# Optimization experiments

Hardware: AMD Instinct MI355X
Metric: run time of the kernel (lower is better)

The kernel has to match this reference:

```python
import jax, jax.numpy as jnp
import numpy as np

VECT = 300   # word-vector dim
H = 128      # GRU hidden size
NSTACK = 3   # MultiHead stacks (shared SelfAttention weights)
SEQ = 4096


def _ln(x, g, b, eps=1e-5):
    m = jnp.mean(x, axis=-1, keepdims=True)
    v = jnp.mean((x - m) ** 2, axis=-1, keepdims=True)
    return g * (x - m) / jnp.sqrt(v + eps) + b


def _multihead(x, q_w, q_b, k_w, k_b, v_w, v_b, aln_g, aln_b, w_w, w_b, mln_g, mln_b):
    # x: [S, 300]. Same attention weights reused for all 3 stacks (as in source).
    scale = jnp.sqrt(jnp.asarray(float(VECT), x.dtype))
    out = x
    for _ in range(NSTACK):
        q = out @ q_w.T + q_b
        k = out @ k_w.T + k_b
        v = out @ v_w.T + v_b
        a = jax.nn.softmax((q @ k.T) / scale, axis=1)      # [S, S]
        h = _ln(a @ v + out, aln_g, aln_b)                  # SelfAttention out
        out = _ln(h @ w_w.T + w_b + x, mln_g, mln_b)        # residual to original x
    return out


def _gru(xs, w_ih, w_hh, b_ih, b_hh):
    # xs: [S, VECT]; PyTorch GRUCell math, h0 = zeros. Input projections batched.
    gx = xs @ w_ih.T + b_ih  # [S, 3H]
    def step(h, g):
        gh = h @ w_hh.T + b_hh
        r = jax.nn.sigmoid(g[:H] + gh[:H])
        z = jax.nn.sigmoid(g[H:2 * H] + gh[H:2 * H])
        n = jnp.tanh(g[2 * H:] + r * gh[2 * H:])
        return (1.0 - z) * n + z * h, None
    h, _ = jax.lax.scan(step, jnp.zeros((H,), xs.dtype), gx)
    return h


def setup_inputs() -> dict:
    key = jax.random.key(0)
    ks = jax.random.split(key, 16)

    def lin(k, o, i, s=0.05):
        k1, k2 = jax.random.split(k)
        return (jax.random.normal(k1, (o, i), jnp.float32) * s,
                jax.random.normal(k2, (o,), jnp.float32) * s)

    q_w, q_b = lin(ks[0], VECT, VECT)
    k_w, k_b = lin(ks[1], VECT, VECT)
    v_w, v_b = lin(ks[2], VECT, VECT)
    w_w, w_b = lin(ks[3], VECT, VECT)
    g1_wih, g1_bih = lin(ks[4], 3 * H, VECT)
    g1_whh, g1_bhh = lin(ks[5], 3 * H, H)
    g2_wih, g2_bih = lin(ks[6], 3 * H, VECT)
    g2_whh, g2_bhh = lin(ks[7], 3 * H, H)
    fc1_w, fc1_b = lin(ks[8], 256, 2 * H)
    fc2_w, fc2_b = lin(ks[9], 3, 256)

    return {
        'x1': jax.random.normal(ks[10], (SEQ, VECT), jnp.float32),
        'x2': jax.random.normal(ks[11], (SEQ, VECT), jnp.float32),
        'q_w': q_w, 'q_b': q_b, 'k_w': k_w, 'k_b': k_b, 'v_w': v_w, 'v_b': v_b,
        'aln_g': jnp.ones((VECT,), jnp.float32), 'aln_b': jnp.zeros((VECT,), jnp.float32),
        'w_w': w_w, 'w_b': w_b,
        'mln_g': jnp.ones((VECT,), jnp.float32), 'mln_b': jnp.zeros((VECT,), jnp.float32),
        'g1_wih': g1_wih, 'g1_whh': g1_whh, 'g1_bih': g1_bih, 'g1_bhh': g1_bhh,
        'g2_wih': g2_wih, 'g2_whh': g2_whh, 'g2_bih': g2_bih, 'g2_bhh': g2_bhh,
        'fc1_w': fc1_w, 'fc1_b': fc1_b, 'fc2_w': fc2_w, 'fc2_b': fc2_b,
    }


def reference(x1, x2, q_w, q_b, k_w, k_b, v_w, v_b, aln_g, aln_b, w_w, w_b,
              mln_g, mln_b, g1_wih, g1_whh, g1_bih, g1_bhh,
              g2_wih, g2_whh, g2_bih, g2_bhh, fc1_w, fc1_b, fc2_w, fc2_b):
    a1 = _multihead(x1, q_w, q_b, k_w, k_b, v_w, v_b, aln_g, aln_b, w_w, w_b, mln_g, mln_b)
    a2 = _multihead(x2, q_w, q_b, k_w, k_b, v_w, v_b, aln_g, aln_b, w_w, w_b, mln_g, mln_b)
    h1 = _gru(a1, g1_wih, g1_whh, g1_bih, g1_bhh)  # [H]
    h2 = _gru(a2, g2_wih, g2_whh, g2_bih, g2_bhh)  # [H]
    h = jnp.concatenate([h1, h2])[None, :]          # [1, 2H]
    h = jax.nn.relu(h @ fc1_w.T + fc1_b)
    return jax.nn.log_softmax(h @ fc2_w.T + fc2_b, axis=1)  # [1, 3]
```

## Files before the change

kernel.cpp:

```cpp
#include <hip/hip_runtime.h>
#include <hip/hip_bf16.h>

#define SEQL 4096
#define VECT 300
#define DP   320
#define NQT  20
#define HN   128
#define G3   384
#define JC   4
#define KROW 328
#define VROW 40
#define PROW 40

typedef unsigned short u16;
typedef unsigned char  u8;
typedef __attribute__((ext_vector_type(8))) short bf16x8;
typedef __attribute__((ext_vector_type(4))) float f32x4;
typedef __attribute__((ext_vector_type(4))) unsigned int u32x4;
typedef __attribute__((ext_vector_type(8))) int   v8i;

#define MFMA(a,b,c) __builtin_amdgcn_mfma_f32_16x16x32_bf16(a,b,c,0,0,0)

#define L2E 1.44269504088896f

__device__ __forceinline__ float bf2f(u16 v){
    union { unsigned u; float f; } t; t.u = ((unsigned)v) << 16; return t.f;
}
__device__ __forceinline__ u16 f2bf(float f){
    union { float f; unsigned u; } t; t.f = f;
    return (u16)((t.u + 0x7FFFu + ((t.u >> 16) & 1u)) >> 16);
}
__device__ __forceinline__ float sigm_f(float x){
    return __builtin_amdgcn_rcpf(1.f + __builtin_amdgcn_exp2f(-L2E * x));
}
__device__ __forceinline__ float tanh_f(float x){
    return fmaf(2.f, __builtin_amdgcn_rcpf(1.f + __builtin_amdgcn_exp2f(-2.f * L2E * x)), -1.f);
}
__device__ __forceinline__ float sel4(f32x4 v, int r){
    float a = (r & 1) ? v.y : v.x;
    float b = (r & 1) ? v.w : v.z;
    return (r & 2) ? b : a;
}

__global__ __launch_bounds__(256) void cvt_pad(const float* __restrict__ src,
                                               u16* __restrict__ dst,
                                               int R, int C, int Rp, int Cp, float scale)
{
    int n = Rp * Cp;
    for (int i = blockIdx.x * blockDim.x + threadIdx.x; i < n; i += gridDim.x * blockDim.x){
        int r = i / Cp, c = i - r * Cp;
        float v = (r < R && c < C) ? src[r * C + c] * scale : 0.f;
        dst[i] = f2bf(v);
    }
}

__global__ __launch_bounds__(256) void cvt_whh(const float* __restrict__ src,
                                               u8* __restrict__ dst)
{
    int idx = blockIdx.x * 256 + threadIdx.x;
    if (idx >= G3 * HN) return;
    int prow = idx >> 7, col = idx & 127;
    int w  = prow / 96, rem = prow - w * 96;
    int tg = rem / 48;  rem -= tg * 48;
    int g  = rem >> 4;  int rr = rem & 15;
    int orow = g * 128 + w * 32 + tg * 16 + rr;
    int pk = __builtin_amdgcn_cvt_pk_fp8_f32(src[orow * HN + col], 0.f, 0, false);
    dst[idx] = (u8)(pk & 0xFF);
}

__global__ __launch_bounds__(256) void scale_copy(const float* __restrict__ src,
                                                  float* __restrict__ dst, int n, float scale)
{
    int i = blockIdx.x * blockDim.x + threadIdx.x;
    if (i < n) dst[i] = src[i] * scale;
}

__global__ __launch_bounds__(256) void pad_x(const float* __restrict__ src,
                                             float* __restrict__ xf, u16* __restrict__ cur)
{
    int n = SEQL * DP;
    for (int i = blockIdx.x * blockDim.x + threadIdx.x; i < n; i += gridDim.x * blockDim.x){
        int r = i / DP, c = i - r * DP;
        float v = (c < VECT) ? src[r * VECT + c] : 0.f;
        xf[i]  = v;
        cur[i] = f2bf(v);
    }
}

template<int NT, int OM, bool WPERSEQ>
__global__ __launch_bounds__(256) void gemm_k(
    const u16* __restrict__ A, const u16* __restrict__ Wp,
    const float* __restrict__ b0, const float* __restrict__ b1, const float* __restrict__ b2,
    int nb, void* __restrict__ Out)
{
    const int lane = threadIdx.x & 63;
    const int wid  = threadIdx.x >> 6;
    const int s    = blockIdx.z;
    const int sl   = blockIdx.y;
    const int wsel = WPERSEQ ? s : sl;
    const int row0 = blockIdx.x * 64 + wid * 16;
    const int m    = lane & 15;
    const int q    = lane >> 4;

    const u16* Arow = A + ((long)s * SEQL + row0) * DP;
    const u16* W    = Wp + (long)wsel * (NT * 16) * DP;

    f32x4 zf = {0.f, 0.f, 0.f, 0.f};
    f32x4 acc[NT];
    #pragma unroll
    for (int n = 0; n < NT; n++) acc[n] = zf;

    for (int c = 0; c < DP / 32; ++c){
        const int koff = c * 32 + q * 8;
        bf16x8 a0 = *(const bf16x8*)(Arow + m * DP + koff);
        #pragma unroll
        for (int n = 0; n < NT; n++){
            bf16x8 b = *(const bf16x8*)(W + (n * 16 + m) * DP + koff);
            acc[n] = MFMA(a0, b, acc[n]);
        }
    }

    const int bsel = WPERSEQ ? s : sl;
    const float* bp = (bsel == 0) ? b0 : ((bsel == 1) ? b1 : b2);
    const long SLC = 2L * SEQL * DP;

    #pragma unroll
    for (int n = 0; n < NT; n++){
        int col = n * 16 + m;
        float bv = (col < nb) ? bp[col] : 0.f;
        #pragma unroll
        for (int r = 0; r < 4; r++){
            long row = row0 + q * 4 + r;
            float v = acc[n][r] + bv;
            if (OM == 1){
                long off = ((long)s * SEQL + row) * (long)(NT * 16) + col;
                ((float*)Out)[off] = v;
            } else if (OM == 4){
                int g = col >> 7, i2 = col & 127;
                long off = ((long)s * SEQL + row) * (long)(NT * 16) + (i2 * 3 + g);
                ((float*)Out)[off] = v;
            } else {
                long off;
                if (sl < 2) off = ((long)(sl * 2 + s) * SEQL + row) * DP + col;
                else        off = 2 * SLC + ((long)s * DP + col) * SEQL + row;
                ((u16*)Out)[off] = f2bf(v);
            }
        }
    }
}

__global__ __launch_bounds__(256, 1) void flash_k(
    const u16* __restrict__ Q, const u16* __restrict__ K, const u16* __restrict__ VT,
    u16* __restrict__ Onum, float* __restrict__ Lp)
{
    const int tid  = threadIdx.x;
    const int lane = tid & 63;
    const int wid  = tid >> 6;
    const int bid  = blockIdx.x;
    const int s    = bid & 1;
    const int jc   = (bid >> 1) & 3;
    const int xi   = bid >> 3;
    const int row0 = xi * 128 + wid * 32;
    const int m = lane & 15, q = lane >> 4;

    __shared__ __align__(16) u16 Kt[32 * KROW];
    __shared__ __align__(16) u16 Vt[DP * VROW];
    __shared__ __align__(16) u16 pb[4][2][16 * PROW];

    const u16* Qb = Q  + ((long)s * SEQL + row0) * DP;
    const u16* Kc = K  + (long)s * SEQL * DP + (long)jc * 1024 * DP;
    const u16* Vc = VT + (long)s * DP * SEQL + jc * 1024;

    bf16x8 qf0[10], qf1[10];
    #pragma unroll
    for (int c = 0; c < 10; c++){
        qf0[c] = *(const bf16x8*)(Qb + (m     ) * DP + c * 32 + q * 8);
        qf1[c] = *(const bf16x8*)(Qb + (m + 16) * DP + c * 32 + q * 8);
    }

    int skoff[5], wkoff[5], svoff[5], wvoff[5];
    #pragma unroll
    for (int it = 0; it < 5; it++){
        int f  = (it * 256 + tid) * 8;
        int rk = f / 320, ck = f - rk * 320;
        skoff[it] = f;
        wkoff[it] = rk * KROW + ck;
        int rv = f >> 5, cv = f & 31;
        svoff[it] = rv * SEQL + cv;
        wvoff[it] = rv * VROW + cv;
    }

    f32x4 zf = {0.f, 0.f, 0.f, 0.f};
    f32x4 oacc0[NQT], oacc1[NQT];
    #pragma unroll
    for (int n = 0; n < NQT; n++){ oacc0[n] = zf; oacc1[n] = zf; }
    float lacc0[4] = {0,0,0,0}, lacc1[4] = {0,0,0,0};

    const float K2 = 0.057735026918962576f * L2E;
    const float MB = -16.f * L2E;

    u32x4 kreg[5], vreg[5];
    #pragma unroll
    for (int it = 0; it < 5; it++){
        kreg[it] = *(const u32x4*)(Kc + skoff[it]);
        vreg[it] = *(const u32x4*)(Vc + svoff[it]);
    }
    #pragma unroll
    for (int it = 0; it < 5; it++){
        *(u32x4*)(&Kt[wkoff[it]]) = kreg[it];
        *(u32x4*)(&Vt[wvoff[it]]) = vreg[it];
    }
    __syncthreads();

    u16* pb0 = &pb[wid][0][0];
    u16* pb1 = &pb[wid][1][0];

    for (int j = 0; j < 32; ++j){
        if (j + 1 < 32){
            const u16* Kj = Kc + (j + 1) * 32 * DP;
            const u16* Vj = Vc + (j + 1) * 32;
            #pragma unroll
            for (int it = 0; it < 5; it++){
                kreg[it] = *(const u32x4*)(Kj + skoff[it]);
                vreg[it] = *(const u32x4*)(Vj + svoff[it]);
            }
        }
        f32x4 s0A = zf, s0B = zf, s1A = zf, s1B = zf;
        #pragma unroll
        for (int c = 0; c < 10; c++){
            bf16x8 kA = *(const bf16x8*)(&Kt[(m     ) * KROW + c * 32 + q * 8]);
            bf16x8 kB = *(const bf16x8*)(&Kt[(m + 16) * KROW + c * 32 + q * 8]);
            s0A = MFMA(qf0[c], kA, s0A);
            s0B = MFMA(qf0[c], kB, s0B);
            s1A = MFMA(qf1[c], kA, s1A);
            s1B = MFMA(qf1[c], kB, s1B);
        }
        #pragma unroll
        for (int r = 0; r < 4; r++){
            float a0 = __builtin_amdgcn_exp2f(fmaf(s0A[r], K2, MB));
            float b0 = __builtin_amdgcn_exp2f(fmaf(s0B[r], K2, MB));
            float a1 = __builtin_amdgcn_exp2f(fmaf(s1A[r], K2, MB));
            float b1 = __builtin_amdgcn_exp2f(fmaf(s1B[r], K2, MB));
            lacc0[r] += a0 + b0;
            lacc1[r] += a1 + b1;
            pb0[(q * 4 + r) * PROW +      m] = f2bf(a0);
            pb0[(q * 4 + r) * PROW + 16 + m] = f2bf(b0);
            pb1[(q * 4 + r) * PROW +      m] = f2bf(a1);
            pb1[(q * 4 + r) * PROW + 16 + m] = f2bf(b1);
        }
        bf16x8 pf0 = *(const bf16x8*)(&pb0[m * PROW + q * 8]);
        bf16x8 pf1 = *(const bf16x8*)(&pb1[m * PROW + q * 8]);
        #pragma unroll
        for (int n = 0; n < NQT; n++){
            bf16x8 vb = *(const bf16x8*)(&Vt[(n * 16 + m) * VROW + q * 8]);
            oacc0[n] = MFMA(pf0, vb, oacc0[n]);
            oacc1[n] = MFMA(pf1, vb, oacc1[n]);
        }
        __syncthreads();
        if (j + 1 < 32){
            #pragma unroll
            for (int it = 0; it < 5; it++){
                *(u32x4*)(&Kt[wkoff[it]]) = kreg[it];
                *(u32x4*)(&Vt[wvoff[it]]) = vreg[it];
            }
        }
        __syncthreads();
    }

    #pragma unroll
    for (int r = 0; r < 4; r++){
        float t0 = lacc0[r], t1 = lacc1[r];
        t0 += __shfl_xor(t0, 1); t0 += __shfl_xor(t0, 2);
        t0 += __shfl_xor(t0, 4); t0 += __shfl_xor(t0, 8);
        t1 += __shfl_xor(t1, 1); t1 += __shfl_xor(t1, 2);
        t1 += __shfl_xor(t1, 4); t1 += __shfl_xor(t1, 8);
        lacc0[r] = t0; lacc1[r] = t1;
    }
    const long grow0 = (long)s * SEQL + row0;
    if (m == 0){
        #pragma unroll
        for (int r = 0; r < 4; r++){
            Lp[(long)jc * 2 * SEQL + grow0 +      q * 4 + r] = lacc0[r];
            Lp[(long)jc * 2 * SEQL + grow0 + 16 + q * 4 + r] = lacc1[r];
        }
    }
    u16* Ob = Onum + ((long)jc * 2 * SEQL + grow0) * DP;
    #pragma unroll
    for (int n = 0; n < NQT; n++)
        #pragma unroll
        for (int r = 0; r < 4; r++){
            Ob[(long)(     q * 4 + r) * DP + n * 16 + m] = f2bf(oacc0[n][r]);
            Ob[(long)(16 + q * 4 + r) * DP + n * 16 + m] = f2bf(oacc1[n][r]);
        }
}

__global__ __launch_bounds__(256) void lncomb_k(const u16* __restrict__ Onum, const float* __restrict__ Lp,
                                                const float* __restrict__ XF,
                                                const float* __restrict__ g, const float* __restrict__ b,
                                                u16* __restrict__ OutB)
{
    long row = (long)((blockIdx.x * blockDim.x + threadIdx.x) >> 6);
    int lane = threadIdx.x & 63;
    if (row >= 2L * SEQL) return;
    float l = 0.f;
    #pragma unroll
    for (int jc = 0; jc < JC; jc++) l += Lp[(long)jc * 2 * SEQL + row];
    float inv = 1.f / l;
    const float* xr = XF + row * DP;
    float v[5], sum = 0.f, sq = 0.f;
    #pragma unroll
    for (int i = 0; i < 5; i++){
        int c = lane + i * 64;
        float o = 0.f;
        #pragma unroll
        for (int jc = 0; jc < JC; jc++)
            o += bf2f(Onum[((long)jc * 2 * SEQL + row) * DP + c]);
        float t = (c < VECT) ? (o * inv + xr[c]) : 0.f;
        v[i] = t; sum += t; sq += t * t;
    }
    #pragma unroll
    for (int o = 1; o < 64; o <<= 1){ sum += __shfl_xor(sum, o); sq += __shfl_xor(sq, o); }
    float mean = sum / VECT;
    float var  = sq / VECT - mean * mean;
    float rstd = rsqrtf(var + 1e-5f);
    #pragma unroll
    for (int i = 0; i < 5; i++){
        int c = lane + i * 64;
        float t = (c < VECT) ? ((v[i] - mean) * rstd * g[c] + b[c]) : 0.f;
        OutB[row * DP + c] = f2bf(t);
    }
}

__global__ __launch_bounds__(256) void ln_k(const float* __restrict__ Xf,
                                            const float* __restrict__ Res0, const float* __restrict__ Res1,
                                            int rstride,
                                            const float* __restrict__ g, const float* __restrict__ b,
                                            u16* __restrict__ OutB, float* __restrict__ OutF)
{
    long row = (long)((blockIdx.x * blockDim.x + threadIdx.x) >> 6);
    int lane = threadIdx.x & 63;
    if (row >= 2L * SEQL) return;
    const float* xr = Xf + row * DP;
    const float* rr = (row < SEQL) ? (Res0 + row * (long)rstride)
                                   : (Res1 + (row - SEQL) * (long)rstride);
    float v[5], sum = 0.f, sq = 0.f;
    #pragma unroll
    for (int i = 0; i < 5; i++){
        int c = lane + i * 64;
        float t = (c < VECT) ? (xr[c] + rr[c]) : 0.f;
        v[i] = t; sum += t; sq += t * t;
    }
    #pragma unroll
    for (int o = 1; o < 64; o <<= 1){ sum += __shfl_xor(sum, o); sq += __shfl_xor(sq, o); }
    float mean = sum / VECT;
    float var  = sq / VECT - mean * mean;
    float rstd = rsqrtf(var + 1e-5f);
    #pragma unroll
    for (int i = 0; i < 5; i++){
        int c = lane + i * 64;
        float t = (c < VECT) ? ((v[i] - mean) * rstd * g[c] + b[c]) : 0.f;
        OutB[row * DP + c] = f2bf(t);
        if (OutF) OutF[row * DP + c] = t;
    }
}

__global__ __launch_bounds__(256, 1) void gru_k(
    const float* __restrict__ GXP,
    const u8* __restrict__ Whh8p,
    const float* __restrict__ Bhh1, const float* __restrict__ Bhh2,
    float* __restrict__ Hout)
{
    const int s = blockIdx.x;
    const int tid = threadIdx.x;
    const int lane = tid & 63;
    const int wid  = tid >> 6;
    const int m = lane & 15, q = lane >> 4;
    const u8* Whh = Whh8p + (long)s * G3 * HN;
    const float* Bhh = s ? Bhh2 : Bhh1;
    const float* gx = GXP + (long)s * SEQL * G3;

    __shared__ __align__(8) u8 hst[2][HN];

    v8i af[6];
    #pragma unroll
    for (int tg = 0; tg < 2; tg++)
        #pragma unroll
        for (int g = 0; g < 3; g++)
            af[tg * 3 + g] = *(const v8i*)(Whh + (long)(wid * 96 + tg * 48 + g * 16 + m) * HN + q * 32);

    const int tgl  = (m >> 2) & 1;
    const int rsel = m & 3;
    const int il   = wid * 32 + tgl * 16 + q * 4 + rsel;
    const int il3  = il * 3;
    const float bhr = Bhh[il], bhz = Bhh[HN + il], bhn = Bhh[2 * HN + il];

    if (tid < HN){ hst[0][tid] = 0; hst[1][tid] = 0; }

    const float* ga = gx + il3;
    float cr0 = ga[0], cz0 = ga[1], cn0 = ga[2];
    const float* gb = gx + G3 + il3;
    float cr1 = gb[0], cz1 = gb[1], cn1 = gb[2];

    __syncthreads();

    float h = 0.f;
    const f32x4 zf = {0.f, 0.f, 0.f, 0.f};

#define GRU_STEP(T, CR, CZ, CN, WB, RB)                                               \
    {                                                                                 \
        v8i bfrag = *(const v8i*)(&hst[RB][q * 32]);                                  \
        f32x4 a0 = __builtin_amdgcn_mfma_scale_f32_16x16x128_f8f6f4(af[0], bfrag, zf, 0, 0, 0, 127, 0, 127); \
        f32x4 a1 = __builtin_amdgcn_mfma_scale_f32_16x16x128_f8f6f4(af[1], bfrag, zf, 0, 0, 0, 127, 0, 127); \
        f32x4 a2 = __builtin_amdgcn_mfma_scale_f32_16x16x128_f8f6f4(af[2], bfrag, zf, 0, 0, 0, 127, 0, 127); \
        f32x4 a3 = __builtin_amdgcn_mfma_scale_f32_16x16x128_f8f6f4(af[3], bfrag, zf, 0, 0, 0, 127, 0, 127); \
        f32x4 a4 = __builtin_amdgcn_mfma_scale_f32_16x16x128_f8f6f4(af[4], bfrag, zf, 0, 0, 0, 127, 0, 127); \
        f32x4 a5 = __builtin_amdgcn_mfma_scale_f32_16x16x128_f8f6f4(af[5], bfrag, zf, 0, 0, 0, 127, 0, 127); \
        float ghr = sel4(tgl ? a3 : a0, rsel);                                        \
        float ghz = sel4(tgl ? a4 : a1, rsel);                                        \
        float ghn = sel4(tgl ? a5 : a2, rsel);                                        \
        float rg = sigm_f(CR + ghr + bhr);                                            \
        float zg = sigm_f(CZ + ghz + bhz);                                            \
        float ng = tanh_f(CN + rg * (ghn + bhn));                                     \
        h = (1.f - zg) * ng + zg * h;                                                 \
        if (m < 8){                                                                   \
            int pk = __builtin_amdgcn_cvt_pk_fp8_f32(h, h, 0, false);                 \
            hst[WB][il] = (u8)(pk & 0xFF);                                            \
        }                                                                             \
        int tp = ((T) + 2 < SEQL) ? (T) + 2 : SEQL - 1;                               \
        const float* gp = gx + (long)tp * G3 + il3;                                   \
        CR = gp[0]; CZ = gp[1]; CN = gp[2];                                           \
        asm volatile("s_waitcnt lgkmcnt(0)" ::: "memory");                            \
        __builtin_amdgcn_s_barrier();                                                 \
        asm volatile("" ::: "memory");                                                \
    }

    for (int t = 0; t < SEQL; t += 2){
        GRU_STEP(t,     cr0, cz0, cn0, 0, 1);
        GRU_STEP(t + 1, cr1, cz1, cn1, 1, 0);
    }
#undef GRU_STEP

    if (m < 8) Hout[s * HN + il] = h;
}

__global__ __launch_bounds__(256) void final_k(const float* __restrict__ Hout,
                                               const float* __restrict__ fc1w, const float* __restrict__ fc1b,
                                               const float* __restrict__ fc2w, const float* __restrict__ fc2b,
                                               float* __restrict__ out)
{
    __shared__ float hb[256];
    __shared__ float r1[256];
    __shared__ float lg[3];
    int tid = threadIdx.x;
    hb[tid] = Hout[tid];
    __syncthreads();
    float a = 0.f;
    for (int k2 = 0; k2 < 256; k2++) a += hb[k2] * fc1w[tid * 256 + k2];
    a += fc1b[tid];
    r1[tid] = fmaxf(a, 0.f);
    __syncthreads();
    if (tid < 3){
        float v = 0.f;
        for (int k2 = 0; k2 < 256; k2++) v += r1[k2] * fc2w[tid * 256 + k2];
        lg[tid] = v + fc2b[tid];
    }
    __syncthreads();
    if (tid == 0){
        float mx = fmaxf(lg[0], fmaxf(lg[1], lg[2]));
        float se = __expf(lg[0] - mx) + __expf(lg[1] - mx) + __expf(lg[2] - mx);
        float ls = mx + logf(se);
        out[0] = lg[0] - ls;
        out[1] = lg[1] - ls;
        out[2] = lg[2] - ls;
    }
}

extern "C" void kernel_launch(void* const* d_in, const int* in_sizes, int n_in,
                              void* d_out, int out_size, void* d_ws, size_t ws_size,
                              hipStream_t stream)
{
    (void)in_sizes; (void)n_in; (void)out_size; (void)ws_size;
    const float* x1     = (const float*)d_in[0];
    const float* x2     = (const float*)d_in[1];
    const float* q_w    = (const float*)d_in[2],  *q_b   = (const float*)d_in[3];
    const float* k_w    = (const float*)d_in[4],  *k_b   = (const float*)d_in[5];
    const float* v_w    = (const float*)d_in[6],  *v_b   = (const float*)d_in[7];
    const float* aln_g  = (const float*)d_in[8],  *aln_b = (const float*)d_in[9];
    const float* w_w    = (const float*)d_in[10], *w_b   = (const float*)d_in[11];
    const float* mln_g  = (const float*)d_in[12], *mln_b = (const float*)d_in[13];
    const float* g1_wih = (const float*)d_in[14], *g1_whh = (const float*)d_in[15];
    const float* g1_bih = (const float*)d_in[16], *g1_bhh = (const float*)d_in[17];
    const float* g2_wih = (const float*)d_in[18], *g2_whh = (const float*)d_in[19];
    const float* g2_bih = (const float*)d_in[20], *g2_bhh = (const float*)d_in[21];
    const float* fc1w   = (const float*)d_in[22], *fc1b  = (const float*)d_in[23];
    const float* fc2w   = (const float*)d_in[24], *fc2b  = (const float*)d_in[25];

    char* wsp = (char*)d_ws;
    auto alloc = [&](size_t bytes) -> char* {
        char* p = wsp; wsp += (bytes + 255) & ~(size_t)255; return p;
    };
    float* XF   = (float*)alloc(2L * SEQL * DP * 4);
    u16*   CUR  = (u16*)  alloc(2L * SEQL * DP * 2);
    u16*   Hb   = (u16*)  alloc(2L * SEQL * DP * 2);
    u16*   Wpk  = (u16*)  alloc(4L * DP * DP * 2);
    u16*   GWpk = (u16*)  alloc(2L * G3 * DP * 2);
    u8*    Whh8 = (u8*)   alloc(2L * G3 * HN);
    float* qbS  = (float*)alloc(DP * 4);
    float* Hout = (float*)alloc(2L * HN * 4);
    float* Lp   = (float*)alloc((long)JC * 2 * SEQL * 4);
    size_t u1 = (2L * 2 * SEQL * DP + 2L * DP * SEQL) * 2;
    size_t u1b = 2L * SEQL * G3 * 4;
    u16*   QKV  = (u16*)  alloc(u1 > u1b ? u1 : u1b);
    u16*   VT   = QKV + 2L * 2 * SEQL * DP;
    float* GX   = (float*)QKV;
    size_t u2 = (long)JC * 2 * SEQL * DP * 2;
    size_t u2b = 2L * SEQL * DP * 4;
    u16*   Onum = (u16*)  alloc(u2 > u2b ? u2 : u2b);
    float* Of   = (float*)Onum;

    pad_x<<<256, 256, 0, stream>>>(x1, XF,                  CUR);
    pad_x<<<256, 256, 0, stream>>>(x2, XF + (long)SEQL*DP,  CUR + (long)SEQL*DP);
    cvt_pad<<<128, 256, 0, stream>>>(q_w, Wpk,                VECT, VECT, DP, DP, 1.f);
    cvt_pad<<<128, 256, 0, stream>>>(k_w, Wpk + 1L * DP * DP, VECT, VECT, DP, DP, 1.f);
    cvt_pad<<<128, 256, 0, stream>>>(v_w, Wpk + 2L * DP * DP, VECT, VECT, DP, DP, 1.f);
    cvt_pad<<<128, 256, 0, stream>>>(w_w, Wpk + 3L * DP * DP, VECT, VECT, DP, DP, 1.f);
    cvt_pad<<<128, 256, 0, stream>>>(g1_wih, GWpk,                 G3, VECT, G3, DP, 1.f);
    cvt_pad<<<128, 256, 0, stream>>>(g2_wih, GWpk + (long)G3 * DP, G3, VECT, G3, DP, 1.f);
    cvt_whh<<<192, 256, 0, stream>>>(g1_whh, Whh8);
    cvt_whh<<<192, 256, 0, stream>>>(g2_whh, Whh8 + (long)G3 * HN);
    scale_copy<<<2, 256, 0, stream>>>(q_b, qbS, VECT, 1.f);

    for (int st = 0; st < 3; ++st){
        gemm_k<NQT, 3, false><<<dim3(SEQL / 64, 3, 2), 256, 0, stream>>>(
            CUR, Wpk, qbS, k_b, v_b, VECT, QKV);
        flash_k<<<dim3(256), 256, 0, stream>>>(QKV, QKV + 2L*SEQL*DP, VT, Onum, Lp);
        lncomb_k<<<dim3(2 * SEQL / 4), 256, 0, stream>>>(Onum, Lp, XF, aln_g, aln_b, Hb);
        gemm_k<NQT, 1, false><<<dim3(SEQL / 64, 1, 2), 256, 0, stream>>>(
            Hb, Wpk + 3L * DP * DP, w_b, nullptr, nullptr, VECT, Of);
        ln_k<<<dim3(2 * SEQL / 4), 256, 0, stream>>>(Of, x1, x2, VECT, mln_g, mln_b, CUR, XF);
    }

    gemm_k<24, 4, true><<<dim3(SEQL / 64, 1, 2), 256, 0, stream>>>(
        CUR, GWpk, g1_bih, g2_bih, nullptr, G3, GX);
    gru_k<<<dim3(2), 256, 0, stream>>>(GX, Whh8, g1_bhh, g2_bhh, Hout);
    final_k<<<dim3(1), 256, 0, stream>>>(Hout, fc1w, fc1b, fc2w, fc2b, (float*)d_out);
}
```

Before: 2.101 ms.

## Fuse output GEMM with LayerNorm, batch prep kernels, lighten flash barriers

Merges the W projection GEMM with the residual add and LayerNorm into one kernel, so each stack no longer writes the fp32 intermediate and launches a separate LN pass. The weight and input preparation launches are folded into a few kernels indexed by blockIdx.y, and the no-op q-bias copy is dropped. In flash_k, __syncthreads is replaced by a raw barrier that waits only on LDS counters. That barrier relies on global loads not needing to complete at the sync point, which is correct here only because the prefetched registers are consumed after the barrier.

Measured after the change: 2.026 ms. -3.6%, faster.

```diff
diff --git a/kernel.cpp b/kernel.cpp
--- a/kernel.cpp
+++ b/kernel.cpp
@@ -23,6 +23,12 @@
 
 #define L2E 1.44269504088896f
 
+#define RAW_BAR() do {                                          \
+    asm volatile("s_waitcnt lgkmcnt(0)" ::: "memory");          \
+    __builtin_amdgcn_s_barrier();                               \
+    asm volatile("" ::: "memory");                              \
+} while (0)
+
 __device__ __forceinline__ float bf2f(u16 v){
     union { unsigned u; float f; } t; t.u = ((unsigned)v) << 16; return t.f;
 }
@@ -42,21 +48,57 @@
     return (r & 2) ? b : a;
 }
 
-__global__ __launch_bounds__(256) void cvt_pad(const float* __restrict__ src,
-                                               u16* __restrict__ dst,
-                                               int R, int C, int Rp, int Cp, float scale)
-{
-    int n = Rp * Cp;
+__global__ __launch_bounds__(256) void pad_x2(const float* __restrict__ x1, const float* __restrict__ x2,
+                                              float* __restrict__ xf, u16* __restrict__ cur)
+{
+    int s = blockIdx.y;
+    const float* src = s ? x2 : x1;
+    float* xfo = xf + (long)s * SEQL * DP;
+    u16*  cro = cur + (long)s * SEQL * DP;
+    int n = SEQL * DP;
     for (int i = blockIdx.x * blockDim.x + threadIdx.x; i < n; i += gridDim.x * blockDim.x){
-        int r = i / Cp, c = i - r * Cp;
-        float v = (r < R && c < C) ? src[r * C + c] * scale : 0.f;
+        int r = i / DP, c = i - r * DP;
+        float v = (c < VECT) ? src[r * VECT + c] : 0.f;
+        xfo[i] = v;
+        cro[i] = f2bf(v);
+    }
+}
+
+__global__ __launch_bounds__(256) void cvt_pad_w4(const float* __restrict__ w0, const float* __restrict__ w1,
+                                                  const float* __restrict__ w2, const float* __restrict__ w3,
+                                                  u16* __restrict__ Wpk)
+{
+    int sl = blockIdx.y;
+    const float* src = (sl == 0) ? w0 : (sl == 1) ? w1 : (sl == 2) ? w2 : w3;
+    u16* dst = Wpk + (long)sl * DP * DP;
+    int n = DP * DP;
+    for (int i = blockIdx.x * blockDim.x + threadIdx.x; i < n; i += gridDim.x * blockDim.x){
+        int r = i / DP, c = i - r * DP;
+        float v = (r < VECT && c < VECT) ? src[r * VECT + c] : 0.f;
         dst[i] = f2bf(v);
     }
 }
 
-__global__ __launch_bounds__(256) void cvt_whh(const float* __restrict__ src,
-                                               u8* __restrict__ dst)
-{
+__global__ __launch_bounds__(256) void cvt_pad_g2(const float* __restrict__ w0, const float* __restrict__ w1,
+                                                  u16* __restrict__ GWpk)
+{
+    int s = blockIdx.y;
+    const float* src = s ? w1 : w0;
+    u16* dst = GWpk + (long)s * G3 * DP;
+    int n = G3 * DP;
+    for (int i = blockIdx.x * blockDim.x + threadIdx.x; i < n; i += gridDim.x * blockDim.x){
+        int r = i / DP, c = i - r * DP;
+        float v = (c < VECT) ? src[r * VECT + c] : 0.f;
+        dst[i] = f2bf(v);
+    }
+}
+
+__global__ __launch_bounds__(256) void cvt_whh2(const float* __restrict__ w0, const float* __restrict__ w1,
+                                                u8* __restrict__ dst0)
+{
+    int s = blockIdx.y;
+    const float* src = s ? w1 : w0;
+    u8* dst = dst0 + (long)s * G3 * HN;
     int idx = blockIdx.x * 256 + threadIdx.x;
     if (idx >= G3 * HN) return;
     int prow = idx >> 7, col = idx & 127;
@@ -68,25 +110,6 @@
     dst[idx] = (u8)(pk & 0xFF);
 }
 
-__global__ __launch_bounds__(256) void scale_copy(const float* __restrict__ src,
-                                                  float* __restrict__ dst, int n, float scale)
-{
-    int i = blockIdx.x * blockDim.x + threadIdx.x;
-    if (i < n) dst[i] = src[i] * scale;
-}
-
-__global__ __launch_bounds__(256) void pad_x(const float* __restrict__ src,
-                                             float* __restrict__ xf, u16* __restrict__ cur)
-{
-    int n = SEQL * DP;
-    for (int i = blockIdx.x * blockDim.x + threadIdx.x; i < n; i += gridDim.x * blockDim.x){
-        int r = i / DP, c = i - r * DP;
-        float v = (c < VECT) ? src[r * VECT + c] : 0.f;
-        xf[i]  = v;
-        cur[i] = f2bf(v);
-    }
-}
-
 template<int NT, int OM, bool WPERSEQ>
 __global__ __launch_bounds__(256) void gemm_k(
     const u16* __restrict__ A, const u16* __restrict__ Wp,
@@ -132,10 +155,7 @@
         for (int r = 0; r < 4; r++){
             long row = row0 + q * 4 + r;
             float v = acc[n][r] + bv;
-            if (OM == 1){
-                long off = ((long)s * SEQL + row) * (long)(NT * 16) + col;
-                ((float*)Out)[off] = v;
-            } else if (OM == 4){
+            if (OM == 4){
                 int g = col >> 7, i2 = col & 127;
                 long off = ((long)s * SEQL + row) * (long)(NT * 16) + (i2 * 3 + g);
                 ((float*)Out)[off] = v;
@@ -149,6 +169,82 @@
     }
 }
 
+__global__ __launch_bounds__(256) void gemmln_k(
+    const u16* __restrict__ A, const u16* __restrict__ Wp, const float* __restrict__ bias,
+    const float* __restrict__ res0, const float* __restrict__ res1,
+    const float* __restrict__ g, const float* __restrict__ b,
+    u16* __restrict__ OutB, float* __restrict__ OutF)
+{
+    const int lane = threadIdx.x & 63;
+    const int wid  = threadIdx.x >> 6;
+    const int s    = blockIdx.z;
+    const int row0 = blockIdx.x * 64 + wid * 16;
+    const int m    = lane & 15;
+    const int q    = lane >> 4;
+
+    const u16* Arow = A + ((long)s * SEQL + row0) * DP;
+    const float* res = s ? res1 : res0;
+
+    f32x4 zf = {0.f, 0.f, 0.f, 0.f};
+    f32x4 acc[NQT];
+    #pragma unroll
+    for (int n = 0; n < NQT; n++) acc[n] = zf;
+
+    for (int c = 0; c < DP / 32; ++c){
+        const int koff = c * 32 + q * 8;
+        bf16x8 a0 = *(const bf16x8*)(Arow + m * DP + koff);
+        #pragma unroll
+        for (int n = 0; n < NQT; n++){
+            bf16x8 bb = *(const bf16x8*)(Wp + (n * 16 + m) * DP + koff);
+            acc[n] = MFMA(a0, bb, acc[n]);
+        }
+    }
+
+    float sum[4] = {0,0,0,0}, sq[4] = {0,0,0,0};
+    #pragma unroll
+    for (int n = 0; n < NQT; n++){
+        int col = n * 16 + m;
+        float bv = (col < VECT) ? bias[col] : 0.f;
+        #pragma unroll
+        for (int r = 0; r < 4; r++){
+            long row = row0 + q * 4 + r;
+            float rr = (col < VECT) ? res[row * VECT + col] : 0.f;
+            float t = (col < VECT) ? (acc[n][r] + bv + rr) : 0.f;
+            acc[n][r] = t;
+            sum[r] += t; sq[r] += t * t;
+        }
+    }
+    #pragma unroll
+    for (int r = 0; r < 4; r++){
+        float su = sum[r], sv = sq[r];
+        su += __shfl_xor(su, 1); sv += __shfl_xor(sv, 1);
+        su += __shfl_xor(su, 2); sv += __shfl_xor(sv, 2);
+        su += __shfl_xor(su, 4); sv += __shfl_xor(sv, 4);
+        su += __shfl_xor(su, 8); sv += __shfl_xor(sv, 8);
+        sum[r] = su; sq[r] = sv;
+    }
+    float mean[4], rstd[4];
+    #pragma unroll
+    for (int r = 0; r < 4; r++){
+        mean[r] = sum[r] / VECT;
+        float var = sq[r] / VECT - mean[r] * mean[r];
+        rstd[r] = rsqrtf(var + 1e-5f);
+    }
+    #pragma unroll
+    for (int n = 0; n < NQT; n++){
+        int col = n * 16 + m;
+        float gv = (col < VECT) ? g[col] : 0.f;
+        float bv = (col < VECT) ? b[col] : 0.f;
+        #pragma unroll
+        for (int r = 0; r < 4; r++){
+            long row = (long)s * SEQL + row0 + q * 4 + r;
+            float t = (col < VECT) ? ((acc[n][r] - mean[r]) * rstd[r] * gv + bv) : 0.f;
+            OutB[row * DP + col] = f2bf(t);
+            OutF[row * DP + col] = t;
+        }
+    }
+}
+
 __global__ __launch_bounds__(256, 1) void flash_k(
     const u16* __restrict__ Q, const u16* __restrict__ K, const u16* __restrict__ VT,
     u16* __restrict__ Onum, float* __restrict__ Lp)
@@ -210,7 +306,7 @@
         *(u32x4*)(&Kt[wkoff[it]]) = kreg[it];
         *(u32x4*)(&Vt[wvoff[it]]) = vreg[it];
     }
-    __syncthreads();
+    RAW_BAR();
 
     u16* pb0 = &pb[wid][0][0];
     u16* pb1 = &pb[wid][1][0];
@@ -256,7 +352,7 @@
             oacc0[n] = MFMA(pf0, vb, oacc0[n]);
             oacc1[n] = MFMA(pf1, vb, oacc1[n]);
         }
-        __syncthreads();
+        RAW_BAR();
         if (j + 1 < 32){
             #pragma unroll
             for (int it = 0; it < 5; it++){
@@ -264,7 +360,7 @@
                 *(u32x4*)(&Vt[wvoff[it]]) = vreg[it];
             }
         }
-        __syncthreads();
+        RAW_BAR();
     }
 
     #pragma unroll
@@ -328,39 +424,6 @@
         int c = lane + i * 64;
         float t = (c < VECT) ? ((v[i] - mean) * rstd * g[c] + b[c]) : 0.f;
         OutB[row * DP + c] = f2bf(t);
-    }
-}
-
-__global__ __launch_bounds__(256) void ln_k(const float* __restrict__ Xf,
-                                            const float* __restrict__ Res0, const float* __restrict__ Res1,
-                                            int rstride,
-                                            const float* __restrict__ g, const float* __restrict__ b,
-                                            u16* __restrict__ OutB, float* __restrict__ OutF)
-{
-    long row = (long)((blockIdx.x * blockDim.x + threadIdx.x) >> 6);
-    int lane = threadIdx.x & 63;
-    if (row >= 2L * SEQL) return;
-    const float* xr = Xf + row * DP;
-    const float* rr = (row < SEQL) ? (Res0 + row * (long)rstride)
-                                   : (Res1 + (row - SEQL) * (long)rstride);
-    float v[5], sum = 0.f, sq = 0.f;
-    #pragma unroll
-    for (int i = 0; i < 5; i++){
-        int c = lane + i * 64;
-        float t = (c < VECT) ? (xr[c] + rr[c]) : 0.f;
-        v[i] = t; sum += t; sq += t * t;
-    }
-    #pragma unroll
-    for (int o = 1; o < 64; o <<= 1){ sum += __shfl_xor(sum, o); sq += __shfl_xor(sq, o); }
-    float mean = sum / VECT;
-    float var  = sq / VECT - mean * mean;
-    float rstd = rsqrtf(var + 1e-5f);
-    #pragma unroll
-    for (int i = 0; i < 5; i++){
-        int c = lane + i * 64;
-        float t = (c < VECT) ? ((v[i] - mean) * rstd * g[c] + b[c]) : 0.f;
-        OutB[row * DP + c] = f2bf(t);
-        if (OutF) OutF[row * DP + c] = t;
     }
 }
 
@@ -505,7 +568,6 @@
     u16*   Wpk  = (u16*)  alloc(4L * DP * DP * 2);
     u16*   GWpk = (u16*)  alloc(2L * G3 * DP * 2);
     u8*    Whh8 = (u8*)   alloc(2L * G3 * HN);
-    float* qbS  = (float*)alloc(DP * 4);
     float* Hout = (float*)alloc(2L * HN * 4);
     float* Lp   = (float*)alloc((long)JC * 2 * SEQL * 4);
     size_t u1 = (2L * 2 * SEQL * DP + 2L * DP * SEQL) * 2;
@@ -513,31 +575,20 @@
     u16*   QKV  = (u16*)  alloc(u1 > u1b ? u1 : u1b);
     u16*   VT   = QKV + 2L * 2 * SEQL * DP;
     float* GX   = (float*)QKV;
-    size_t u2 = (long)JC * 2 * SEQL * DP * 2;
-    size_t u2b = 2L * SEQL * DP * 4;
-    u16*   Onum = (u16*)  alloc(u2 > u2b ? u2 : u2b);
-    float* Of   = (float*)Onum;
-
-    pad_x<<<256, 256, 0, stream>>>(x1, XF,                  CUR);
-    pad_x<<<256, 256, 0, stream>>>(x2, XF + (long)SEQL*DP,  CUR + (long)SEQL*DP);
-    cvt_pad<<<128, 256, 0, stream>>>(q_w, Wpk,                VECT, VECT, DP, DP, 1.f);
-    cvt_pad<<<128, 256, 0, stream>>>(k_w, Wpk + 1L * DP * DP, VECT, VECT, DP, DP, 1.f);
-    cvt_pad<<<128, 256, 0, stream>>>(v_w, Wpk + 2L * DP * DP, VECT, VECT, DP, DP, 1.f);
-    cvt_pad<<<128, 256, 0, stream>>>(w_w, Wpk + 3L * DP * DP, VECT, VECT, DP, DP, 1.f);
-    cvt_pad<<<128, 256, 0, stream>>>(g1_wih, GWpk,                 G3, VECT, G3, DP, 1.f);
-    cvt_pad<<<128, 256, 0, stream>>>(g2_wih, GWpk + (long)G3 * DP, G3, VECT, G3, DP, 1.f);
-    cvt_whh<<<192, 256, 0, stream>>>(g1_whh, Whh8);
-    cvt_whh<<<192, 256, 0, stream>>>(g2_whh, Whh8 + (long)G3 * HN);
-    scale_copy<<<2, 256, 0, stream>>>(q_b, qbS, VECT, 1.f);
+    u16*   Onum = (u16*)  alloc((long)JC * 2 * SEQL * DP * 2);
+
+    pad_x2<<<dim3(256, 2), 256, 0, stream>>>(x1, x2, XF, CUR);
+    cvt_pad_w4<<<dim3(128, 4), 256, 0, stream>>>(q_w, k_w, v_w, w_w, Wpk);
+    cvt_pad_g2<<<dim3(128, 2), 256, 0, stream>>>(g1_wih, g2_wih, GWpk);
+    cvt_whh2<<<dim3(192, 2), 256, 0, stream>>>(g1_whh, g2_whh, Whh8);
 
     for (int st = 0; st < 3; ++st){
         gemm_k<NQT, 3, false><<<dim3(SEQL / 64, 3, 2), 256, 0, stream>>>(
-            CUR, Wpk, qbS, k_b, v_b, VECT, QKV);
+            CUR, Wpk, q_b, k_b, v_b, VECT, QKV);
         flash_k<<<dim3(256), 256, 0, stream>>>(QKV, QKV + 2L*SEQL*DP, VT, Onum, Lp);
         lncomb_k<<<dim3(2 * SEQL / 4), 256, 0, stream>>>(Onum, Lp, XF, aln_g, aln_b, Hb);
-        gemm_k<NQT, 1, false><<<dim3(SEQL / 64, 1, 2), 256, 0, stream>>>(
-            Hb, Wpk + 3L * DP * DP, w_b, nullptr, nullptr, VECT, Of);
-        ln_k<<<dim3(2 * SEQL / 4), 256, 0, stream>>>(Of, x1, x2, VECT, mln_g, mln_b, CUR, XF);
+        gemmln_k<<<dim3(SEQL / 64, 1, 2), 256, 0, stream>>>(
+            Hb, Wpk + 3L * DP * DP, w_b, x1, x2, mln_g, mln_b, CUR, XF);
     }
 
     gemm_k<24, 4, true><<<dim3(SEQL / 64, 1, 2), 256, 0, stream>>>(
```
